# Performance work log

Hardware: AMD Instinct MI355X
Metric: run time of the kernel (lower is better)

The kernel has to match this reference:

```python
import jax, jax.numpy as jnp
import numpy as np

B, S, H = 2, 2048, 1024
NH, NKV, HD = 16, 4, 64
G, R = NKV, NH // NKV  # 4 kv groups, 4 query heads per group


def setup_inputs() -> dict:
    key = jax.random.key(0)
    ks = jax.random.split(key, 7)
    scale = 1.0 / np.sqrt(H)
    return {
        "hidden_states": jax.random.normal(ks[0], (B, S, H), jnp.float32),
        "cos": jax.random.normal(ks[1], (S, HD), jnp.float32),
        "sin": jax.random.normal(ks[2], (S, HD), jnp.float32),
        "attention_mask": jnp.ones((B, S), jnp.float32),
        "Wq": jax.random.normal(ks[3], (H, NH * HD), jnp.float32) * scale,
        "Wk": jax.random.normal(ks[4], (H, NKV * HD), jnp.float32) * scale,
        "Wv": jax.random.normal(ks[5], (H, NKV * HD), jnp.float32) * scale,
        "Wo": jax.random.normal(ks[6], (NH * HD, H), jnp.float32) * scale,
    }


def _rotate_half(x):
    h = x.shape[-1] // 2
    return jnp.concatenate([-x[..., h:], x[..., :h]], axis=-1)


def reference(hidden_states, cos, sin, attention_mask, Wq, Wk, Wv, Wo):
    x = hidden_states
    q = (x @ Wq).reshape(B, S, NH, HD)
    k = (x @ Wk).reshape(B, S, NKV, HD)
    v = (x @ Wv).reshape(B, S, NKV, HD)
    # RoPE: cos/sin [S,HD] broadcast over batch and heads
    c = cos[None, :, None, :]
    s = sin[None, :, None, :]
    q = q * c + _rotate_half(q) * s
    k = k * c + _rotate_half(k) * s
    # GQA without materializing repeated KV: q grouped as [B,S,G,R,HD]
    qg = q.reshape(B, S, G, R, HD)
    scores = jnp.einsum("bsgrd,btgd->bgrst", qg, k) / np.sqrt(HD)  # [B,G,R,S,T]
    causal = jnp.tril(jnp.ones((S, S), bool))
    scores = jnp.where(causal[None, None, None], scores, -jnp.inf)
    scores = scores + ((1.0 - attention_mask) * -1e9)[:, None, None, None, :]
    probs = jax.nn.softmax(scores.astype(jnp.float32), axis=-1).astype(q.dtype)
    out = jnp.einsum("bgrst,btgd->bsgrd", probs, v).reshape(B, S, NH * HD)
    return out @ Wo
```

## Files before the change

### kernel.cpp

```cpp
#include <hip/hip_runtime.h>
#include <math.h>

#define B_   2
#define S_   2048
#define H_   1024
#define NH_  16
#define NKV_ 4
#define HD_  64
#define R_   (NH_ / NKV_)
#define QKVW 1536

typedef __attribute__((ext_vector_type(8))) short bf16x8;
typedef __attribute__((ext_vector_type(4))) float f32x4;

__device__ inline short f2bf(float f) {
    unsigned u = __float_as_uint(f);
    u += 0x7FFF + ((u >> 16) & 1);
    return (short)(u >> 16);
}

__device__ inline void gload_lds16(const void* gptr, void* lptr) {
    __builtin_amdgcn_global_load_lds(
        (const __attribute__((address_space(1))) unsigned int*)gptr,
        (__attribute__((address_space(3))) unsigned int*)lptr,
        16, 0, 0);
}

__global__ __launch_bounds__(256) void tconv_all(const float* __restrict__ Wq,
                                                 const float* __restrict__ Wk,
                                                 const float* __restrict__ Wv,
                                                 const float* __restrict__ Wo,
                                                 short* __restrict__ Wqkvt,
                                                 short* __restrict__ Wot,
                                                 const float* __restrict__ x,
                                                 short* __restrict__ xb) {
    const int bx = blockIdx.x;
    const int tid = threadIdx.x;

    if (bx >= 640) {
        const size_t e0 = (size_t)(bx - 640) * 16384;
#pragma unroll
        for (int t = 0; t < 8; t++) {
            const size_t i = e0 + ((size_t)t * 256 + tid) * 8;
            float4 a = *(const float4*)&x[i];
            float4 c = *(const float4*)&x[i + 4];
            bf16x8 o;
            o[0] = f2bf(a.x); o[1] = f2bf(a.y); o[2] = f2bf(a.z); o[3] = f2bf(a.w);
            o[4] = f2bf(c.x); o[5] = f2bf(c.y); o[6] = f2bf(c.z); o[7] = f2bf(c.w);
            *(bf16x8*)&xb[i] = o;
        }
        return;
    }

    __shared__ short T[64][68];
    const float* W; short* Wt; int N, idx;
    if (bx < 256)      { W = Wq; Wt = Wqkvt;                     N = 1024; idx = bx; }
    else if (bx < 320) { W = Wk; Wt = Wqkvt + 1024 * 1024;       N = 256;  idx = bx - 256; }
    else if (bx < 384) { W = Wv; Wt = Wqkvt + 1280 * 1024;       N = 256;  idx = bx - 320; }
    else               { W = Wo; Wt = Wot;                       N = 1024; idx = bx - 384; }
    const int ntiles = N >> 6;
    const int n0 = (idx % ntiles) * 64;
    const int k0 = (idx / ntiles) * 64;

    const int r  = tid >> 4;
    const int c4 = (tid & 15) * 4;
#pragma unroll
    for (int t = 0; t < 4; t++) {
        int row = t * 16 + r;
        float4 v = *(const float4*)&W[(size_t)(k0 + row) * N + n0 + c4];
        T[c4 + 0][row] = f2bf(v.x);
        T[c4 + 1][row] = f2bf(v.y);
        T[c4 + 2][row] = f2bf(v.z);
        T[c4 + 3][row] = f2bf(v.w);
    }
    __syncthreads();
#pragma unroll
    for (int t = 0; t < 4; t++) {
        int row = t * 16 + r;
        short4 o = *(short4*)&T[row][c4];
        *(short4*)&Wt[(size_t)(n0 + row) * 1024 + k0 + c4] = o;
    }
}

__global__ __launch_bounds__(256) void gemm1_fused(const short* __restrict__ xb,
                                                   const short* __restrict__ Bt,
                                                   short* __restrict__ qkv,
                                                   short* __restrict__ Vtg,
                                                   const float* __restrict__ cosb,
                                                   const float* __restrict__ sinb) {
    __shared__ short Ah[128 * 32];
    __shared__ short Bh[128 * 32];

    const int tid  = threadIdx.x;
    const int w    = tid >> 6;
    const int lane = tid & 63;
    const int ln   = lane & 15;
    const int qd   = lane >> 4;
    const int wr   = w >> 1, wc = w & 1;
    const int row0 = blockIdx.y * 128;
    const int col0 = blockIdx.x * 128;

    const int sr = lane >> 2;
    const int sk = (lane & 3) * 8;

    f32x4 acc[4][4];
#pragma unroll
    for (int mi = 0; mi < 4; mi++)
#pragma unroll
        for (int ni = 0; ni < 4; ni++)
            acc[mi][ni] = (f32x4){0.f, 0.f, 0.f, 0.f};

    for (int k0 = 0; k0 < 1024; k0 += 32) {
        __syncthreads();
        gload_lds16(xb + (size_t)(row0 + w * 16 + sr) * 1024 + k0 + sk,      &Ah[(w * 16) * 32]);
        gload_lds16(xb + (size_t)(row0 + 64 + w * 16 + sr) * 1024 + k0 + sk, &Ah[(64 + w * 16) * 32]);
        gload_lds16(Bt + (size_t)(col0 + w * 16 + sr) * 1024 + k0 + sk,      &Bh[(w * 16) * 32]);
        gload_lds16(Bt + (size_t)(col0 + 64 + w * 16 + sr) * 1024 + k0 + sk, &Bh[(64 + w * 16) * 32]);
        __syncthreads();

        bf16x8 af[4], bf[4];
#pragma unroll
        for (int mi = 0; mi < 4; mi++)
            af[mi] = *(const bf16x8*)&Ah[(wr * 64 + mi * 16 + ln) * 32 + qd * 8];
#pragma unroll
        for (int ni = 0; ni < 4; ni++)
            bf[ni] = *(const bf16x8*)&Bh[(wc * 64 + ni * 16 + ln) * 32 + qd * 8];
#pragma unroll
        for (int mi = 0; mi < 4; mi++)
#pragma unroll
            for (int ni = 0; ni < 4; ni++)
                acc[mi][ni] = __builtin_amdgcn_mfma_f32_16x16x32_bf16(af[mi], bf[ni], acc[mi][ni], 0, 0, 0);
    }

    const int colw = col0 + wc * 64;
    if (colw < H_ + NKV_ * HD_) {
#pragma unroll
        for (int mi = 0; mi < 4; mi++)
#pragma unroll
            for (int i = 0; i < 4; i++) {
                const int row  = row0 + wr * 64 + mi * 16 + qd * 4 + i;
                const int spos = row & (S_ - 1);
                const float* cp = cosb + (size_t)spos * HD_;
                const float* sp = sinb + (size_t)spos * HD_;
                float o0[4];
#pragma unroll
                for (int ni = 0; ni < 2; ni++) {
                    const int d = ni * 16 + ln;
                    float x0 = acc[mi][ni][i], x1 = acc[mi][ni + 2][i];
                    o0[ni]     = x0 * cp[d]      - x1 * sp[d];
                    o0[ni + 2] = x1 * cp[d + 32] + x0 * sp[d + 32];
                }
                short* Cp = qkv + (size_t)row * QKVW + colw + ln;
#pragma unroll
                for (int ni = 0; ni < 4; ni++) Cp[ni * 16] = f2bf(o0[ni]);
            }
    } else {
        const int g = (colw - (H_ + NKV_ * HD_)) >> 6;
#pragma unroll
        for (int mi = 0; mi < 4; mi++) {
            const int rbase = row0 + wr * 64 + mi * 16 + qd * 4;
            const int bg = ((rbase >> 11) * NKV_) + g;
            const int s0 = rbase & (S_ - 1);
#pragma unroll
            for (int ni = 0; ni < 4; ni++) {
                const int d = ni * 16 + ln;
                short4 pk = { f2bf(acc[mi][ni][0]), f2bf(acc[mi][ni][1]),
                              f2bf(acc[mi][ni][2]), f2bf(acc[mi][ni][3]) };
                *(short4*)&Vtg[((size_t)bg * HD_ + d) * S_ + s0] = pk;
            }
        }
    }
}

__global__ __launch_bounds__(256) void gemm2_bt(const short* __restrict__ A, int lda,
                                                const short* __restrict__ Bt,
                                                float* __restrict__ C, int ldc,
                                                int K) {
    __shared__ short Ah[128 * 32];
    __shared__ short Bh[128 * 32];

    const int tid  = threadIdx.x;
    const int w    = tid >> 6;
    const int lane = tid & 63;
    const int ln   = lane & 15;
    const int qd   = lane >> 4;
    const int wr   = w >> 1, wc = w & 1;
    const int row0 = blockIdx.y * 128;
    const int col0 = blockIdx.x * 128;

    const int sr = lane >> 2;
    const int sk = (lane & 3) * 8;

    f32x4 acc[4][4];
#pragma unroll
    for (int mi = 0; mi < 4; mi++)
#pragma unroll
        for (int ni = 0; ni < 4; ni++)
            acc[mi][ni] = (f32x4){0.f, 0.f, 0.f, 0.f};

    for (int k0 = 0; k0 < K; k0 += 32) {
        __syncthreads();
        gload_lds16(A + (size_t)(row0 + w * 16 + sr) * lda + k0 + sk,      &Ah[(w * 16) * 32]);
        gload_lds16(A + (size_t)(row0 + 64 + w * 16 + sr) * lda + k0 + sk, &Ah[(64 + w * 16) * 32]);
        gload_lds16(Bt + (size_t)(col0 + w * 16 + sr) * K + k0 + sk,       &Bh[(w * 16) * 32]);
        gload_lds16(Bt + (size_t)(col0 + 64 + w * 16 + sr) * K + k0 + sk,  &Bh[(64 + w * 16) * 32]);
        __syncthreads();

        bf16x8 af[4], bf[4];
#pragma unroll
        for (int mi = 0; mi < 4; mi++)
            af[mi] = *(const bf16x8*)&Ah[(wr * 64 + mi * 16 + ln) * 32 + qd * 8];
#pragma unroll
        for (int ni = 0; ni < 4; ni++)
            bf[ni] = *(const bf16x8*)&Bh[(wc * 64 + ni * 16 + ln) * 32 + qd * 8];
#pragma unroll
        for (int mi = 0; mi < 4; mi++)
#pragma unroll
            for (int ni = 0; ni < 4; ni++)
                acc[mi][ni] = __builtin_amdgcn_mfma_f32_16x16x32_bf16(af[mi], bf[ni], acc[mi][ni], 0, 0, 0);
    }

#pragma unroll
    for (int mi = 0; mi < 4; mi++)
#pragma unroll
        for (int i = 0; i < 4; i++) {
            const size_t row = row0 + wr * 64 + mi * 16 + qd * 4 + i;
            float* Cp = C + row * ldc + col0 + wc * 64 + ln;
#pragma unroll
            for (int ni = 0; ni < 4; ni++) Cp[ni * 16] = acc[mi][ni][i];
        }
}

__global__ __launch_bounds__(512, 2) void attn_kernel(short* __restrict__ qkv,
                                                      const short* __restrict__ Vtg,
                                                      const float* __restrict__ maskb) {
    const int tid  = threadIdx.x;
    const int w    = tid >> 6;
    const int lane = tid & 63;
    const int ln   = lane & 15;
    const int qd   = lane >> 4;

    const int fid = blockIdx.x;
    const int bg  = fid & 7;
    const int u   = fid >> 3;
    const int b   = bg >> 2;
    const int g   = bg & 3;
    const int h   = g * R_ + (u & 3);
    const int a   = u >> 2;

    __shared__ short Ks[2][64 * 72];
    __shared__ short Vt[2][64 * 72];
    __shared__ short Ps[8][16 * 72];
    __shared__ float mskS[2][64];
    short* const ps = Ps[w];

    const short* const Kb = qkv + (size_t)b * S_ * QKVW + H_ + g * HD_;
    const short* const Vb = Vtg + (size_t)bg * HD_ * S_;
    const float* const mb = maskb + b * S_;

    const int fr = tid >> 3;
    const int fc = (tid & 7) * 8;

#pragma unroll 1
    for (int ph = 0; ph < 2; ph++) {
        const int qt   = ph ? (15 - a) : a;
        const int rowb = qt * 128 + w * 16;
        const int ktd  = 2 * qt + (w >> 2);
        const int ntp  = 2 * qt + 2;
        const int qrow = rowb + ln;

        bf16x8 qf0, qf1;
        {
            const short* qp = qkv + (size_t)(b * S_ + rowb + ln) * QKVW + h * HD_;
            qf0 = *(const bf16x8*)&qp[qd * 8];
            qf1 = *(const bf16x8*)&qp[32 + qd * 8];
        }

        f32x4 O[4] = {};
        float mrow = -1e30f, lrow = 0.0f;

        *(bf16x8*)&Ks[0][fr * 72 + fc] = *(const bf16x8*)&Kb[(size_t)fr * QKVW + fc];
        *(bf16x8*)&Vt[0][fr * 72 + fc] = *(const bf16x8*)&Vb[(size_t)fr * S_ + fc];
        if (tid < 64) mskS[0][tid] = (1.0f - mb[tid]) * -1e9f;
        __syncthreads();

        int cur = 0;
#pragma unroll 1
        for (int kt = 0; kt < ntp; kt++) {
            const int base = kt * 64;
            const bool pf = (kt + 1 < ntp);

            bf16x8 pk, pv;
            float pm = 0.0f;
            if (pf) {
                const int nb = base + 64;
                pk = *(const bf16x8*)&Kb[(size_t)(nb + fr) * QKVW + fc];
                pv = *(const bf16x8*)&Vb[(size_t)fr * S_ + nb + fc];
                if (tid < 64) pm = (1.0f - mb[nb + tid]) * -1e9f;
            }

            if (kt <= ktd) {
                f32x4 St[4];
#pragma unroll
                for (int kg = 0; kg < 4; kg++) {
                    bf16x8 ka0 = *(const bf16x8*)&Ks[cur][(kg * 16 + ln) * 72 + qd * 8];
                    bf16x8 ka1 = *(const bf16x8*)&Ks[cur][(kg * 16 + ln) * 72 + 32 + qd * 8];
                    f32x4 z = {0.f, 0.f, 0.f, 0.f};
                    z = __builtin_amdgcn_mfma_f32_16x16x32_bf16(ka0, qf0, z, 0, 0, 0);
                    St[kg] = __builtin_amdgcn_mfma_f32_16x16x32_bf16(ka1, qf1, z, 0, 0, 0);
                }

                bf16x8 vb[2][4];
#pragma unroll
                for (int kc2 = 0; kc2 < 2; kc2++)
#pragma unroll
                    for (int dt = 0; dt < 4; dt++)
                        vb[kc2][dt] = *(const bf16x8*)&Vt[cur][(dt * 16 + ln) * 72 + kc2 * 32 + qd * 8];

                float sc[4][4];
#pragma unroll
                for (int kg = 0; kg < 4; kg++) {
                    float4 mv = *(const float4*)&mskS[cur][kg * 16 + qd * 4];
                    sc[kg][0] = fmaf(St[kg][0], 0.125f, mv.x);
                    sc[kg][1] = fmaf(St[kg][1], 0.125f, mv.y);
                    sc[kg][2] = fmaf(St[kg][2], 0.125f, mv.z);
                    sc[kg][3] = fmaf(St[kg][3], 0.125f, mv.w);
                }
                if (kt == ktd) {
#pragma unroll
                    for (int kg = 0; kg < 4; kg++) {
                        const int keyb = base + kg * 16 + qd * 4;
#pragma unroll
                        for (int i = 0; i < 4; i++)
                            if (keyb + i > qrow) sc[kg][i] = -1e30f;
                    }
                }

                float mx = sc[0][0];
#pragma unroll
                for (int kg = 0; kg < 4; kg++)
#pragma unroll
                    for (int i = 0; i < 4; i++) mx = fmaxf(mx, sc[kg][i]);
                mx = fmaxf(mx, __shfl_xor(mx, 16));
                mx = fmaxf(mx, __shfl_xor(mx, 32));

                if (__ballot(mx > mrow + 8.0f)) {
                    float nm    = fmaxf(mrow, mx);
                    float alpha = __expf(mrow - nm);
                    lrow *= alpha;
#pragma unroll
                    for (int i = 0; i < 4; i++) {
                        float av = __shfl(alpha, qd * 4 + i);
#pragma unroll
                        for (int dt = 0; dt < 4; dt++) O[dt][i] *= av;
                    }
                    mrow = nm;
                }
                const float nm = mrow;

                float ls = 0.0f;
#pragma unroll
                for (int kg = 0; kg < 4; kg++)
#pragma unroll
                    for (int i = 0; i < 4; i++) {
                        float p = __expf(sc[kg][i] - nm);
                        sc[kg][i] = p;
                        ls += p;
                    }
                ls += __shfl_xor(ls, 16);
                ls += __shfl_xor(ls, 32);
                lrow += ls;

#pragma unroll
                for (int kg = 0; kg < 4; kg++) {
                    short4 pko = { f2bf(sc[kg][0]), f2bf(sc[kg][1]),
                                   f2bf(sc[kg][2]), f2bf(sc[kg][3]) };
                    *(short4*)&ps[ln * 72 + kg * 16 + qd * 4] = pko;
                }

#pragma unroll
                for (int kc2 = 0; kc2 < 2; kc2++) {
                    bf16x8 pa = *(const bf16x8*)&ps[ln * 72 + kc2 * 32 + qd * 8];
#pragma unroll
                    for (int dt = 0; dt < 4; dt++)
                        O[dt] = __builtin_amdgcn_mfma_f32_16x16x32_bf16(pa, vb[kc2][dt], O[dt], 0, 0, 0);
                }
            }

            if (pf) {
                const int nxt = cur ^ 1;
                *(bf16x8*)&Ks[nxt][fr * 72 + fc] = pk;
                *(bf16x8*)&Vt[nxt][fr * 72 + fc] = pv;
                if (tid < 64) mskS[nxt][tid] = pm;
            }
            __syncthreads();
            cur ^= 1;
        }

#pragma unroll
        for (int i = 0; i < 4; i++) {
            float li  = __shfl(lrow, qd * 4 + i);
            float inv = 1.0f / li;
            const int row = rowb + qd * 4 + i;
            short* op = qkv + (size_t)(b * S_ + row) * QKVW + h * HD_ + ln;
#pragma unroll
            for (int dt = 0; dt < 4; dt++) op[dt * 16] = f2bf(O[dt][i] * inv);
        }
    }
}

extern "C" void kernel_launch(void* const* d_in, const int* in_sizes, int n_in,
                              void* d_out, int out_size, void* d_ws, size_t ws_size,
                              hipStream_t stream) {
    const float* x     = (const float*)d_in[0];
    const float* cosb  = (const float*)d_in[1];
    const float* sinb  = (const float*)d_in[2];
    const float* maskb = (const float*)d_in[3];
    const float* Wq    = (const float*)d_in[4];
    const float* Wk    = (const float*)d_in[5];
    const float* Wv    = (const float*)d_in[6];
    const float* Wo    = (const float*)d_in[7];

    const int M = B_ * S_;

    short* qkv   = (short*)d_ws;
    short* Wqkvt = qkv + (size_t)M * QKVW;
    short* Wot   = Wqkvt + (size_t)QKVW * H_;
    short* Vtg   = Wot + (size_t)H_ * H_;
    short* xb    = (short*)d_out;
    float* out   = (float*)d_out;

    dim3 blk(256);

    tconv_all<<<dim3(896), blk, 0, stream>>>(Wq, Wk, Wv, Wo, Wqkvt, Wot, x, xb);

    gemm1_fused<<<dim3(QKVW / 128, M / 128), blk, 0, stream>>>(xb, Wqkvt, qkv, Vtg, cosb, sinb);

    attn_kernel<<<dim3(256), dim3(512), 0, stream>>>(qkv, Vtg, maskb);

    gemm2_bt<<<dim3(H_ / 128, M / 128), blk, 0, stream>>>(qkv, QKVW, Wot, out, H_, H_);
}
```

Measured before the change: 195.0 us.

## Shrink GEMM M-tiles to 64 and use exp2 with packed bf16 in attention

Both projection GEMMs move from 128x128 to 64x128 output tiles, which doubles the grid so more blocks fill the CUs, at the cost of less operand reuse per block. The attention softmax folds log2(e) into the score scale and mask so it can call the hardware exp2 directly, with the rescale threshold adjusted to match. Probabilities are converted with the packed v_cvt_pk_bf16_f32 instruction instead of manual rounding. Together these aim to cut softmax ALU work and improve GEMM occupancy.

```diff
diff --git a/kernel.cpp b/kernel.cpp
--- a/kernel.cpp
+++ b/kernel.cpp
@@ -18,6 +18,22 @@
     u += 0x7FFF + ((u >> 16) & 1);
     return (short)(u >> 16);
 }
+
+__device__ inline float exp2fast(float x) {
+#if __has_builtin(__builtin_amdgcn_exp2f)
+    return __builtin_amdgcn_exp2f(x);
+#else
+    float r; asm volatile("v_exp_f32 %0, %1\n\ts_nop 1" : "=v"(r) : "v"(x)); return r;
+#endif
+}
+
+__device__ inline unsigned cvt_pk_bf16(float lo, float hi) {
+    unsigned r;
+    asm("v_cvt_pk_bf16_f32 %0, %1, %2" : "=v"(r) : "v"(lo), "v"(hi));
+    return r;
+}
+
+#define LOG2E 1.4426950408889634f
 
 __device__ inline void gload_lds16(const void* gptr, void* lptr) {
     __builtin_amdgcn_global_load_lds(
@@ -88,7 +104,7 @@
                                                    short* __restrict__ Vtg,
                                                    const float* __restrict__ cosb,
                                                    const float* __restrict__ sinb) {
-    __shared__ short Ah[128 * 32];
+    __shared__ short Ah[64 * 32];
     __shared__ short Bh[128 * 32];
 
     const int tid  = threadIdx.x;
@@ -97,15 +113,15 @@
     const int ln   = lane & 15;
     const int qd   = lane >> 4;
     const int wr   = w >> 1, wc = w & 1;
-    const int row0 = blockIdx.y * 128;
+    const int row0 = blockIdx.y * 64;
     const int col0 = blockIdx.x * 128;
 
     const int sr = lane >> 2;
     const int sk = (lane & 3) * 8;
 
-    f32x4 acc[4][4];
-#pragma unroll
-    for (int mi = 0; mi < 4; mi++)
+    f32x4 acc[2][4];
+#pragma unroll
+    for (int mi = 0; mi < 2; mi++)
 #pragma unroll
         for (int ni = 0; ni < 4; ni++)
             acc[mi][ni] = (f32x4){0.f, 0.f, 0.f, 0.f};
@@ -113,32 +129,31 @@
     for (int k0 = 0; k0 < 1024; k0 += 32) {
         __syncthreads();
         gload_lds16(xb + (size_t)(row0 + w * 16 + sr) * 1024 + k0 + sk,      &Ah[(w * 16) * 32]);
-        gload_lds16(xb + (size_t)(row0 + 64 + w * 16 + sr) * 1024 + k0 + sk, &Ah[(64 + w * 16) * 32]);
-        gload_lds16(Bt + (size_t)(col0 + w * 16 + sr) * 1024 + k0 + sk,      &Bh[(w * 16) * 32]);
-        gload_lds16(Bt + (size_t)(col0 + 64 + w * 16 + sr) * 1024 + k0 + sk, &Bh[(64 + w * 16) * 32]);
+        gload_lds16(Bt + (size_t)(col0 + w * 32 + sr) * 1024 + k0 + sk,      &Bh[(w * 32) * 32]);
+        gload_lds16(Bt + (size_t)(col0 + w * 32 + 16 + sr) * 1024 + k0 + sk, &Bh[(w * 32 + 16) * 32]);
         __syncthreads();
 
-        bf16x8 af[4], bf[4];
-#pragma unroll
-        for (int mi = 0; mi < 4; mi++)
-            af[mi] = *(const bf16x8*)&Ah[(wr * 64 + mi * 16 + ln) * 32 + qd * 8];
+        bf16x8 af[2], bfr[4];
+#pragma unroll
+        for (int mi = 0; mi < 2; mi++)
+            af[mi] = *(const bf16x8*)&Ah[(wr * 32 + mi * 16 + ln) * 32 + qd * 8];
 #pragma unroll
         for (int ni = 0; ni < 4; ni++)
-            bf[ni] = *(const bf16x8*)&Bh[(wc * 64 + ni * 16 + ln) * 32 + qd * 8];
-#pragma unroll
-        for (int mi = 0; mi < 4; mi++)
+            bfr[ni] = *(const bf16x8*)&Bh[(wc * 64 + ni * 16 + ln) * 32 + qd * 8];
+#pragma unroll
+        for (int mi = 0; mi < 2; mi++)
 #pragma unroll
             for (int ni = 0; ni < 4; ni++)
-                acc[mi][ni] = __builtin_amdgcn_mfma_f32_16x16x32_bf16(af[mi], bf[ni], acc[mi][ni], 0, 0, 0);
+                acc[mi][ni] = __builtin_amdgcn_mfma_f32_16x16x32_bf16(af[mi], bfr[ni], acc[mi][ni], 0, 0, 0);
     }
 
     const int colw = col0 + wc * 64;
     if (colw < H_ + NKV_ * HD_) {
 #pragma unroll
-        for (int mi = 0; mi < 4; mi++)
+        for (int mi = 0; mi < 2; mi++)
 #pragma unroll
             for (int i = 0; i < 4; i++) {
-                const int row  = row0 + wr * 64 + mi * 16 + qd * 4 + i;
+                const int row  = row0 + wr * 32 + mi * 16 + qd * 4 + i;
                 const int spos = row & (S_ - 1);
                 const float* cp = cosb + (size_t)spos * HD_;
                 const float* sp = sinb + (size_t)spos * HD_;
@@ -157,8 +172,8 @@
     } else {
         const int g = (colw - (H_ + NKV_ * HD_)) >> 6;
 #pragma unroll
-        for (int mi = 0; mi < 4; mi++) {
-            const int rbase = row0 + wr * 64 + mi * 16 + qd * 4;
+        for (int mi = 0; mi < 2; mi++) {
+            const int rbase = row0 + wr * 32 + mi * 16 + qd * 4;
             const int bg = ((rbase >> 11) * NKV_) + g;
             const int s0 = rbase & (S_ - 1);
 #pragma unroll
@@ -176,7 +191,7 @@
                                                 const short* __restrict__ Bt,
                                                 float* __restrict__ C, int ldc,
                                                 int K) {
-    __shared__ short Ah[128 * 32];
+    __shared__ short Ah[64 * 32];
     __shared__ short Bh[128 * 32];
 
     const int tid  = threadIdx.x;
@@ -185,46 +200,45 @@
     const int ln   = lane & 15;
     const int qd   = lane >> 4;
     const int wr   = w >> 1, wc = w & 1;
-    const int row0 = blockIdx.y * 128;
+    const int row0 = blockIdx.y * 64;
     const int col0 = blockIdx.x * 128;
 
     const int sr = lane >> 2;
     const int sk = (lane & 3) * 8;
 
-    f32x4 acc[4][4];
-#pragma unroll
-    for (int mi = 0; mi < 4; mi++)
+    f32x4 acc[2][4];
+#pragma unroll
+    for (int mi = 0; mi < 2; mi++)
 #pragma unroll
         for (int ni = 0; ni < 4; ni++)
             acc[mi][ni] = (f32x4){0.f, 0.f, 0.f, 0.f};
 
     for (int k0 = 0; k0 < K; k0 += 32) {
         __syncthreads();
-        gload_lds16(A + (size_t)(row0 + w * 16 + sr) * lda + k0 + sk,      &Ah[(w * 16) * 32]);
-        gload_lds16(A + (size_t)(row0 + 64 + w * 16 + sr) * lda + k0 + sk, &Ah[(64 + w * 16) * 32]);
-        gload_lds16(Bt + (size_t)(col0 + w * 16 + sr) * K + k0 + sk,       &Bh[(w * 16) * 32]);
-        gload_lds16(Bt + (size_t)(col0 + 64 + w * 16 + sr) * K + k0 + sk,  &Bh[(64 + w * 16) * 32]);
+        gload_lds16(A + (size_t)(row0 + w * 16 + sr) * lda + k0 + sk, &Ah[(w * 16) * 32]);
+        gload_lds16(Bt + (size_t)(col0 + w * 32 + sr) * K + k0 + sk, &Bh[(w * 32) * 32]);
+        gload_lds16(Bt + (size_t)(col0 + w * 32 + 16 + sr) * K + k0 + sk, &Bh[(w * 32 + 16) * 32]);
         __syncthreads();
 
-        bf16x8 af[4], bf[4];
-#pragma unroll
-        for (int mi = 0; mi < 4; mi++)
-            af[mi] = *(const bf16x8*)&Ah[(wr * 64 + mi * 16 + ln) * 32 + qd * 8];
+        bf16x8 af[2], bfr[4];
+#pragma unroll
+        for (int mi = 0; mi < 2; mi++)
+            af[mi] = *(const bf16x8*)&Ah[(wr * 32 + mi * 16 + ln) * 32 + qd * 8];
 #pragma unroll
         for (int ni = 0; ni < 4; ni++)
-            bf[ni] = *(const bf16x8*)&Bh[(wc * 64 + ni * 16 + ln) * 32 + qd * 8];
-#pragma unroll
-        for (int mi = 0; mi < 4; mi++)
+            bfr[ni] = *(const bf16x8*)&Bh[(wc * 64 + ni * 16 + ln) * 32 + qd * 8];
+#pragma unroll
+        for (int mi = 0; mi < 2; mi++)
 #pragma unroll
             for (int ni = 0; ni < 4; ni++)
-                acc[mi][ni] = __builtin_amdgcn_mfma_f32_16x16x32_bf16(af[mi], bf[ni], acc[mi][ni], 0, 0, 0);
-    }
-
-#pragma unroll
-    for (int mi = 0; mi < 4; mi++)
+                acc[mi][ni] = __builtin_amdgcn_mfma_f32_16x16x32_bf16(af[mi], bfr[ni], acc[mi][ni], 0, 0, 0);
+    }
+
+#pragma unroll
+    for (int mi = 0; mi < 2; mi++)
 #pragma unroll
         for (int i = 0; i < 4; i++) {
-            const size_t row = row0 + wr * 64 + mi * 16 + qd * 4 + i;
+            const size_t row = row0 + wr * 32 + mi * 16 + qd * 4 + i;
             float* Cp = C + row * ldc + col0 + wc * 64 + ln;
 #pragma unroll
             for (int ni = 0; ni < 4; ni++) Cp[ni * 16] = acc[mi][ni][i];
@@ -281,7 +295,7 @@
 
         *(bf16x8*)&Ks[0][fr * 72 + fc] = *(const bf16x8*)&Kb[(size_t)fr * QKVW + fc];
         *(bf16x8*)&Vt[0][fr * 72 + fc] = *(const bf16x8*)&Vb[(size_t)fr * S_ + fc];
-        if (tid < 64) mskS[0][tid] = (1.0f - mb[tid]) * -1e9f;
+        if (tid < 64) mskS[0][tid] = (1.0f - mb[tid]) * (-1e9f * LOG2E);
         __syncthreads();
 
         int cur = 0;
@@ -296,7 +310,7 @@
                 const int nb = base + 64;
                 pk = *(const bf16x8*)&Kb[(size_t)(nb + fr) * QKVW + fc];
                 pv = *(const bf16x8*)&Vb[(size_t)fr * S_ + nb + fc];
-                if (tid < 64) pm = (1.0f - mb[nb + tid]) * -1e9f;
+                if (tid < 64) pm = (1.0f - mb[nb + tid]) * (-1e9f * LOG2E);
             }
 
             if (kt <= ktd) {
@@ -321,10 +335,10 @@
 #pragma unroll
                 for (int kg = 0; kg < 4; kg++) {
                     float4 mv = *(const float4*)&mskS[cur][kg * 16 + qd * 4];
-                    sc[kg][0] = fmaf(St[kg][0], 0.125f, mv.x);
-                    sc[kg][1] = fmaf(St[kg][1], 0.125f, mv.y);
-                    sc[kg][2] = fmaf(St[kg][2], 0.125f, mv.z);
-                    sc[kg][3] = fmaf(St[kg][3], 0.125f, mv.w);
+                    sc[kg][0] = fmaf(St[kg][0], 0.125f * LOG2E, mv.x);
+                    sc[kg][1] = fmaf(St[kg][1], 0.125f * LOG2E, mv.y);
+                    sc[kg][2] = fmaf(St[kg][2], 0.125f * LOG2E, mv.z);
+                    sc[kg][3] = fmaf(St[kg][3], 0.125f * LOG2E, mv.w);
                 }
                 if (kt == ktd) {
 #pragma unroll
@@ -344,9 +358,9 @@
                 mx = fmaxf(mx, __shfl_xor(mx, 16));
                 mx = fmaxf(mx, __shfl_xor(mx, 32));
 
-                if (__ballot(mx > mrow + 8.0f)) {
+                if (__ballot(mx > mrow + 11.5416f)) {
                     float nm    = fmaxf(mrow, mx);
-                    float alpha = __expf(mrow - nm);
+                    float alpha = exp2fast(mrow - nm);
                     lrow *= alpha;
 #pragma unroll
                     for (int i = 0; i < 4; i++) {
@@ -363,7 +377,7 @@
                 for (int kg = 0; kg < 4; kg++)
 #pragma unroll
                     for (int i = 0; i < 4; i++) {
-                        float p = __expf(sc[kg][i] - nm);
+                        float p = exp2fast(sc[kg][i] - nm);
                         sc[kg][i] = p;
                         ls += p;
                     }
@@ -373,9 +387,10 @@
 
 #pragma unroll
                 for (int kg = 0; kg < 4; kg++) {
-                    short4 pko = { f2bf(sc[kg][0]), f2bf(sc[kg][1]),
-                                   f2bf(sc[kg][2]), f2bf(sc[kg][3]) };
-                    *(short4*)&ps[ln * 72 + kg * 16 + qd * 4] = pko;
+                    uint2 pw;
+                    pw.x = cvt_pk_bf16(sc[kg][0], sc[kg][1]);
+                    pw.y = cvt_pk_bf16(sc[kg][2], sc[kg][3]);
+                    *(uint2*)&ps[ln * 72 + kg * 16 + qd * 4] = pw;
                 }
 
 #pragma unroll
@@ -434,9 +449,9 @@
 
     tconv_all<<<dim3(896), blk, 0, stream>>>(Wq, Wk, Wv, Wo, Wqkvt, Wot, x, xb);
 
-    gemm1_fused<<<dim3(QKVW / 128, M / 128), blk, 0, stream>>>(xb, Wqkvt, qkv, Vtg, cosb, sinb);
+    gemm1_fused<<<dim3(QKVW / 128, M / 64), blk, 0, stream>>>(xb, Wqkvt, qkv, Vtg, cosb, sinb);
 
     attn_kernel<<<dim3(256), dim3(512), 0, stream>>>(qkv, Vtg, maskb);
 
-    gemm2_bt<<<dim3(H_ / 128, M / 128), blk, 0, stream>>>(qkv, QKVW, Wot, out, H_, H_);
-}
+    gemm2_bt<<<dim3(H_ / 128, M / 64), blk, 0, stream>>>(qkv, QKVW, Wot, out, H_, H_);
+}
```

Result: faster. 184.4 us (-5.5%).
